# Optimization experiments

Measured on AMD Instinct MI355X. Metric: run time of the kernel, lower is better.

Reference implementation:

```python
import math
import jax, jax.numpy as jnp
import numpy as np

B, NQ, NK, DIM, H, HD = 2, 1024, 2048, 1024, 16, 64


def setup_inputs() -> dict:
    key = jax.random.key(0)
    ks = jax.random.split(key, 12)
    s = 1.0 / math.sqrt(DIM)
    return {
        "q": jax.random.normal(ks[0], (B, NQ, DIM), jnp.float32),
        "k": jax.random.normal(ks[1], (B, NK, DIM), jnp.float32),
        "v": jax.random.normal(ks[2], (B, NK, DIM), jnp.float32),
        "distances": jax.random.uniform(ks[3], (B, NQ, NK), jnp.float32),
        "attn_mask": jax.random.bernoulli(ks[4], 0.5, (B, NQ, NK)),
        "key_padding_mask_q": jax.random.bernoulli(ks[5], 0.5, (B, NQ)),
        "key_padding_mask_k": jax.random.bernoulli(ks[6], 0.5, (B, NK)),
        "Wq": jax.random.normal(ks[7], (H * HD, DIM), jnp.float32) * s,
        "Wk": jax.random.normal(ks[8], (H * HD, DIM), jnp.float32) * s,
        "Wv": jax.random.normal(ks[9], (H * HD, DIM), jnp.float32) * s,
        "Wo": jax.random.normal(ks[10], (DIM, H * HD), jnp.float32) * s,
        "gate_alpha": jnp.float32(0.1),
    }


def reference(q, k, v, distances, attn_mask, key_padding_mask_q,
              key_padding_mask_k, Wq, Wk, Wv, Wo, gate_alpha):
    bsz, q_len, _ = q.shape
    k_len = k.shape[1]
    neg = jnp.finfo(q.dtype).min

    # projections -> (B, H, N, HD)
    qp = (q @ Wq.T).reshape(bsz, q_len, H, HD).transpose(0, 2, 1, 3)
    kp = (k @ Wk.T).reshape(bsz, k_len, H, HD).transpose(0, 2, 1, 3)
    vp = (v @ Wv.T).reshape(bsz, k_len, H, HD).transpose(0, 2, 1, 3)

    scores = jnp.einsum('bhqd,bhkd->bhqk', qp, kp) / math.sqrt(HD)
    scores = jnp.where(attn_mask[:, None, :, :], scores, neg)
    scores = jnp.where(key_padding_mask_k[:, None, None, :], scores, neg)

    attn = jax.nn.softmax(scores, axis=-1)  # (B,H,NQ,NK)

    # distance gating: mask, batch-mean normalize, exponential gate
    d = distances * attn_mask.astype(distances.dtype)
    d = d * key_padding_mask_k[:, None, :].astype(d.dtype)
    mean = d.sum(axis=(-1, -2)) / (q_len * k_len + 1e-6)
    mean = jnp.maximum(mean, 1e-6)[:, None, None]
    d = d / mean
    alpha = jax.nn.softplus(gate_alpha)
    gate = jnp.exp(-alpha * d)[:, None, :, :]  # (B,1,NQ,NK)

    w = attn * gate
    w = w / (w.sum(axis=-1, keepdims=True) + 1e-6)

    out = jnp.einsum('bhqk,bhkd->bhqd', w, vp)
    out = out.transpose(0, 2, 1, 3).reshape(bsz, q_len, H * HD)
    out = out * key_padding_mask_q[:, :, None].astype(out.dtype)
    return out @ Wo.T
```

## Files before the change

### kernel.cpp

```cpp
#include <hip/hip_runtime.h>
#include <hip/hip_bf16.h>
#include <cfloat>

#define B_   2
#define NQ_  1024
#define NK_  2048
#define H_   16
#define HD_  64
#define VPAD 2176
#define GPAD 2112

typedef float  floatx4 __attribute__((ext_vector_type(4)));
typedef __bf16 bf16x8  __attribute__((ext_vector_type(8)));
typedef __bf16 bf16x4  __attribute__((ext_vector_type(4)));

static __device__ __forceinline__ floatx4 mfma16(bf16x8 a, bf16x8 b, floatx4 c) {
    return __builtin_amdgcn_mfma_f32_16x16x32_bf16(a, b, c, 0, 0, 0);
}

static __device__ __forceinline__ void gl_lds(const __bf16* g, __bf16* lbase,
                                              int lane) {
#if __has_builtin(__builtin_amdgcn_global_load_lds)
    __builtin_amdgcn_global_load_lds(
        (const __attribute__((address_space(1))) void*)g,
        (__attribute__((address_space(3))) void*)lbase, 16, 0, 0);
#else
    *(bf16x8*)(lbase + lane * 8) = *(const bf16x8*)g;
#endif
}

struct CvtArgs {
    const float* src[7];
    __bf16*      dst[7];
};

__global__ __launch_bounds__(256) void cvt_mean_kernel(
    CvtArgs a, const float* __restrict__ dist, const int* __restrict__ amask,
    const int* __restrict__ kpmk, float* __restrict__ msum,
    __bf16* __restrict__ dmask)
{
    if (blockIdx.x >= 1792) {
        const int mb = blockIdx.x - 1792;
        const int b  = mb >> 9;
        const float* d  = dist  + (size_t)b * NQ_ * NK_;
        const int*   am = amask + (size_t)b * NQ_ * NK_;
        const int*   km = kpmk  + b * NK_;
        __bf16*      dm = dmask + (size_t)b * NQ_ * GPAD;
        const int base = (mb & 511) * 256 + threadIdx.x;
        float s = 0.f;
        #pragma unroll
        for (int j = 0; j < 4; j++) {
            const int i   = base + j * 131072;
            const int idx = i * 4;
            const int kk  = idx & (NK_ - 1);
            const int q   = i >> 9;
            float4 dv = *(const float4*)(d + idx);
            int4   mv = *(const int4*)(am + idx);
            int4   kv = *(const int4*)(km + kk);
            bf16x4 o;
            if (mv.x && kv.x) { s += dv.x; o[0] = (__bf16)dv.x; } else o[0] = (__bf16)3e38f;
            if (mv.y && kv.y) { s += dv.y; o[1] = (__bf16)dv.y; } else o[1] = (__bf16)3e38f;
            if (mv.z && kv.z) { s += dv.z; o[2] = (__bf16)dv.z; } else o[2] = (__bf16)3e38f;
            if (mv.w && kv.w) { s += dv.w; o[3] = (__bf16)dv.w; } else o[3] = (__bf16)3e38f;
            *(bf16x4*)&dm[(size_t)q * GPAD + kk] = o;
        }
        #pragma unroll
        for (int off = 32; off >= 1; off >>= 1) s += __shfl_down(s, off);
        __shared__ float wsum[4];
        if ((threadIdx.x & 63) == 0) wsum[threadIdx.x >> 6] = s;
        __syncthreads();
        if (threadIdx.x == 0)
            atomicAdd(&msum[b], wsum[0] + wsum[1] + wsum[2] + wsum[3]);
        return;
    }
    #pragma unroll
    for (int j = 0; j < 4; j++) {
        size_t r = (size_t)blockIdx.x * 1024 + j * 256 + threadIdx.x;
        int s;
        if (r < 262144)                  { s = 0; }
        else if ((r -= 262144) < 524288) { s = 1; }
        else if ((r -= 524288) < 524288) { s = 2; }
        else { r -= 524288; s = 3 + (int)(r >> 17); r &= 131071; }
        const float* sp = a.src[s] + r * 8;
        float4 f0 = *(const float4*)sp;
        float4 f1 = *(const float4*)(sp + 4);
        bf16x8 o;
        o[0] = (__bf16)f0.x; o[1] = (__bf16)f0.y; o[2] = (__bf16)f0.z; o[3] = (__bf16)f0.w;
        o[4] = (__bf16)f1.x; o[5] = (__bf16)f1.y; o[6] = (__bf16)f1.z; o[7] = (__bf16)f1.w;
        *(bf16x8*)(a.dst[s] + r * 8) = o;
    }
}

template <typename EPI>
static __device__ __forceinline__ void gemm128_core(
    const __bf16* __restrict__ A, const __bf16* __restrict__ Bw,
    int m0, int n0, __bf16* As, __bf16* Bs, EPI epi)
{
    const int t    = threadIdx.x;
    const int w    = t >> 6, lane = t & 63;
    const int lrow = lane & 15, quad = lane >> 4;
    const int lr   = lane >> 2, lc = lane & 3;

    floatx4 acc[4][4];
    #pragma unroll
    for (int mi = 0; mi < 4; mi++)
        #pragma unroll
        for (int ni = 0; ni < 4; ni++) acc[mi][ni] = floatx4{0.f, 0.f, 0.f, 0.f};

    const __bf16* ga = A  + (size_t)(m0 + w * 32 + lr) * 1024 + lc * 8;
    const __bf16* gb = Bw + (size_t)(n0 + w * 32 + lr) * 1024 + lc * 8;

    for (int k0 = 0; k0 < 1024; k0 += 64) {
        __syncthreads();
        #pragma unroll
        for (int h = 0; h < 2; h++) {
            gl_lds(ga + k0 + h * 32,             &As[h * 4096 + (w * 32) * 32],      lane);
            gl_lds(ga + k0 + h * 32 + 16 * 1024, &As[h * 4096 + (w * 32 + 16) * 32], lane);
            gl_lds(gb + k0 + h * 32,             &Bs[h * 4096 + (w * 32) * 32],      lane);
            gl_lds(gb + k0 + h * 32 + 16 * 1024, &Bs[h * 4096 + (w * 32 + 16) * 32], lane);
        }
        __syncthreads();

        #pragma unroll
        for (int h = 0; h < 2; h++) {
            bf16x8 af[4], bfr[4];
            #pragma unroll
            for (int mi = 0; mi < 4; mi++)
                af[mi] = *(const bf16x8*)
                    &As[h * 4096 + ((w & 1) * 64 + mi * 16 + lrow) * 32 + quad * 8];
            #pragma unroll
            for (int ni = 0; ni < 4; ni++)
                bfr[ni] = *(const bf16x8*)
                    &Bs[h * 4096 + ((w >> 1) * 64 + ni * 16 + lrow) * 32 + quad * 8];
            #pragma unroll
            for (int mi = 0; mi < 4; mi++)
                #pragma unroll
                for (int ni = 0; ni < 4; ni++)
                    acc[mi][ni] = mfma16(af[mi], bfr[ni], acc[mi][ni]);
        }
    }

    #pragma unroll
    for (int mi = 0; mi < 4; mi++)
        #pragma unroll
        for (int ni = 0; ni < 4; ni++)
            #pragma unroll
            for (int r = 0; r < 4; r++) {
                const int m = m0 + (w & 1) * 64 + mi * 16 + quad * 4 + r;
                const int n = n0 + (w >> 1) * 64 + ni * 16 + lrow;
                epi(m, n, acc[mi][ni][r]);
            }
}

template <typename EPI>
static __device__ __forceinline__ void gemm32_core(
    const __bf16* __restrict__ A, const __bf16* __restrict__ Bw,
    int m0, int n0, EPI epi)
{
    __shared__ alignas(16) __bf16 As[2][32 * 32];
    __shared__ alignas(16) __bf16 Bs[2][128 * 32];
    const int t    = threadIdx.x;
    const int w    = t >> 6, lane = t & 63;
    const int lrow = lane & 15, quad = lane >> 4;
    const int lr   = lane >> 2, lc = lane & 3;

    floatx4 acc[2][2];
    #pragma unroll
    for (int mi = 0; mi < 2; mi++)
        #pragma unroll
        for (int ni = 0; ni < 2; ni++) acc[mi][ni] = floatx4{0.f, 0.f, 0.f, 0.f};

    const __bf16* ga = A  + (size_t)(m0 + (w & 1) * 16 + lr) * 1024 + lc * 8;
    const __bf16* gb = Bw + (size_t)(n0 + w * 32 + lr) * 1024 + lc * 8;

    for (int k0 = 0; k0 < 1024; k0 += 64) {
        __syncthreads();
        #pragma unroll
        for (int h = 0; h < 2; h++) {
            if (w < 2)
                gl_lds(ga + k0 + h * 32, &As[h][(w * 16) * 32], lane);
            gl_lds(gb + k0 + h * 32,             &Bs[h][(w * 32) * 32],      lane);
            gl_lds(gb + k0 + h * 32 + 16 * 1024, &Bs[h][(w * 32 + 16) * 32], lane);
        }
        __syncthreads();

        #pragma unroll
        for (int h = 0; h < 2; h++) {
            bf16x8 af[2], bfr[2];
            #pragma unroll
            for (int mi = 0; mi < 2; mi++)
                af[mi] = *(const bf16x8*)
                    &As[h][(mi * 16 + lrow) * 32 + quad * 8];
            #pragma unroll
            for (int ni = 0; ni < 2; ni++)
                bfr[ni] = *(const bf16x8*)
                    &Bs[h][(w * 32 + ni * 16 + lrow) * 32 + quad * 8];
            #pragma unroll
            for (int mi = 0; mi < 2; mi++)
                #pragma unroll
                for (int ni = 0; ni < 2; ni++)
                    acc[mi][ni] = mfma16(af[mi], bfr[ni], acc[mi][ni]);
        }
    }

    #pragma unroll
    for (int mi = 0; mi < 2; mi++)
        #pragma unroll
        for (int ni = 0; ni < 2; ni++)
            #pragma unroll
            for (int r = 0; r < 4; r++) {
                const int m = m0 + mi * 16 + quad * 4 + r;
                const int n = n0 + w * 32 + ni * 16 + lrow;
                epi(m, n, acc[mi][ni][r]);
            }
}

__global__ __launch_bounds__(256) void proj_kernel(
    const __bf16* __restrict__ qb, const __bf16* __restrict__ kb,
    const __bf16* __restrict__ vb, const __bf16* __restrict__ wqb,
    const __bf16* __restrict__ wkb, const __bf16* __restrict__ wvb,
    __bf16* __restrict__ qp, __bf16* __restrict__ kp,
    __bf16* __restrict__ vpT)
{
    __shared__ alignas(16) __bf16 As[2 * 128 * 32];
    __shared__ alignas(16) __bf16 Bs[2 * 128 * 32];
    const int z = blockIdx.z;
    if (z == 0) {
        if ((int)blockIdx.x >= 16) return;
        gemm128_core(qb, wqb, blockIdx.x * 128, blockIdx.y * 128, As, Bs,
                     [&](int m, int n, float v) {
            const int b = m >> 10, q = m & 1023;
            const int h = n >> 6,  d = n & 63;
            qp[(((size_t)(b * 16 + h) * NQ_ + q) << 6) + d] = (__bf16)v;
        });
    } else if (z == 1) {
        gemm128_core(kb, wkb, blockIdx.x * 128, blockIdx.y * 128, As, Bs,
                     [&](int m, int n, float v) {
            const int b = m >> 11, key = m & 2047;
            const int h = n >> 6,  d = n & 63;
            kp[(((size_t)(b * 16 + h) * NK_ + key) << 6) + d] = (__bf16)v;
        });
    } else {
        gemm128_core(wvb, vb, blockIdx.y * 128, blockIdx.x * 128, As, Bs,
                     [&](int m, int n, float v) {
            const int h = m >> 6,  d = m & 63;
            const int b = n >> 11, key = n & 2047;
            vpT[((size_t)(b * 16 + h) * HD_ + d) * VPAD + key] = (__bf16)v;
        });
    }
}

__global__ __launch_bounds__(256) void oproj_kernel(
    const __bf16* __restrict__ A, const __bf16* __restrict__ W,
    float* __restrict__ Cout)
{
    const int m0 = blockIdx.x * 32, n0 = blockIdx.y * 128;
    gemm32_core(A, W, m0, n0, [&](int m, int n, float v) {
        Cout[(size_t)m * 1024 + n] = v;
    });
}

__global__ __launch_bounds__(256, 4) void attn_kernel(
    const __bf16* __restrict__ qp, const __bf16* __restrict__ kp,
    const __bf16* __restrict__ vpT, const __bf16* __restrict__ dmask,
    const float* __restrict__ msum, const float* __restrict__ galpha,
    float* __restrict__ Opart, float* __restrict__ Gpart)
{
    __shared__ __bf16 Ks[64 * 72];
    __shared__ __bf16 Vt[2][64 * 72];
    __shared__ __bf16 Ps[4][16 * 72];
    const int t    = threadIdx.x;
    const int w    = t >> 6, lane = t & 63;
    const int lrow = lane & 15, quad = lane >> 4;
    const int bid  = ((blockIdx.x & 7) << 7) | (blockIdx.x >> 3);
    const int qt   = bid & 15;
    const int bh   = (bid >> 4) & 31;
    const int z    = bid >> 9;
    const int b    = bh >> 4, h = bh & 15;
    const int q0   = qt * 64 + w * 16;
    const int kb0  = z * (NK_ / 2);
    const int NT   = NK_ / 128;

    const float mean  = fmaxf(msum[b] / ((float)(NQ_ * NK_) + 1e-6f), 1e-6f);
    const float alpha = log1pf(__expf(galpha[0]));
    const float cg    = -alpha / mean;

    const __bf16* qb = qp + ((size_t)bh * NQ_ + q0 + lrow) * HD_ + quad * 8;
    const bf16x8 qf0 = *(const bf16x8*)qb;
    const bf16x8 qf1 = *(const bf16x8*)(qb + 32);

    const int srow0 = t >> 3,        sc0 = t & 7;
    const int srow1 = 32 + (t >> 3), sc1 = t & 7;
    const int so0 = srow0 * 72 + sc0 * 8;
    const int so1 = srow1 * 72 + sc1 * 8;
    const __bf16* Kg = kp  + ((size_t)bh * NK_ + kb0) * HD_;
    const __bf16* Vg = vpT + (size_t)bh * HD_ * VPAD + kb0;
    const __bf16* grow = dmask + ((size_t)b * NQ_ + q0 + lrow) * GPAD + kb0;

    float G = 0.f;
    floatx4 O[4];
    #pragma unroll
    for (int nb = 0; nb < 4; nb++) O[nb] = floatx4{0.f, 0.f, 0.f, 0.f};

    bf16x8 kr0, kr1, vr0, vr1;
    bf16x4 gr[4];
    auto loadt = [&](int kb) {
        kr0 = *(const bf16x8*)(Kg + (size_t)(kb + srow0) * HD_ + sc0 * 8);
        kr1 = *(const bf16x8*)(Kg + (size_t)(kb + srow1) * HD_ + sc1 * 8);
        vr0 = *(const bf16x8*)(Vg + (size_t)srow0 * VPAD + kb + sc0 * 8);
        vr1 = *(const bf16x8*)(Vg + (size_t)srow1 * VPAD + kb + sc1 * 8);
        #pragma unroll
        for (int c = 0; c < 4; c++)
            gr[c] = *(const bf16x4*)(grow + kb + c * 16 + quad * 4);
    };
    loadt(0);

    for (int ib = 0; ib < NT; ib++) {
        const int kb  = ib * 64;
        const int cur = ib & 1;

        __syncthreads();
        *(bf16x8*)&Ks[so0]      = kr0;
        *(bf16x8*)&Ks[so1]      = kr1;
        *(bf16x8*)&Vt[cur][so0] = vr0;
        *(bf16x8*)&Vt[cur][so1] = vr1;
        __syncthreads();

        bf16x4 gcur[4];
        #pragma unroll
        for (int c = 0; c < 4; c++) gcur[c] = gr[c];
        if (ib + 1 < NT) loadt(kb + 64);

        __builtin_amdgcn_s_setprio(1);
        floatx4 s4[4];
        #pragma unroll
        for (int c = 0; c < 4; c++) {
            bf16x8 kf0 = *(const bf16x8*)&Ks[(c * 16 + lrow) * 72 + quad * 8];
            bf16x8 kf1 = *(const bf16x8*)&Ks[(c * 16 + lrow) * 72 + 32 + quad * 8];
            floatx4 a = floatx4{0.f, 0.f, 0.f, 0.f};
            a = mfma16(kf0, qf0, a);
            a = mfma16(kf1, qf1, a);
            s4[c] = a;
        }

        if (ib > 0) {
            const int prv = cur ^ 1;
            bf16x8 pf0 = *(const bf16x8*)&Ps[w][lrow * 72 + quad * 8];
            bf16x8 pf1 = *(const bf16x8*)&Ps[w][lrow * 72 + 32 + quad * 8];
            #pragma unroll
            for (int nb = 0; nb < 4; nb++) {
                bf16x8 vf0 = *(const bf16x8*)
                    &Vt[prv][(nb * 16 + lrow) * 72 + quad * 8];
                bf16x8 vf1 = *(const bf16x8*)
                    &Vt[prv][(nb * 16 + lrow) * 72 + 32 + quad * 8];
                O[nb] = mfma16(pf0, vf0, O[nb]);
                O[nb] = mfma16(pf1, vf1, O[nb]);
            }
        }
        __builtin_amdgcn_s_setprio(0);

        #pragma unroll
        for (int c = 0; c < 4; c++) {
            const float e0 = __expf(fmaf(s4[c][0], 0.125f, cg * (float)gcur[c][0]));
            const float e1 = __expf(fmaf(s4[c][1], 0.125f, cg * (float)gcur[c][1]));
            const float e2 = __expf(fmaf(s4[c][2], 0.125f, cg * (float)gcur[c][2]));
            const float e3 = __expf(fmaf(s4[c][3], 0.125f, cg * (float)gcur[c][3]));
            G += (e0 + e1) + (e2 + e3);
            bf16x4 pk;
            pk[0] = (__bf16)e0; pk[1] = (__bf16)e1;
            pk[2] = (__bf16)e2; pk[3] = (__bf16)e3;
            *(bf16x4*)&Ps[w][lrow * 72 + c * 16 + quad * 4] = pk;
        }
    }

    {
        const int prv = (NT - 1) & 1;
        bf16x8 pf0 = *(const bf16x8*)&Ps[w][lrow * 72 + quad * 8];
        bf16x8 pf1 = *(const bf16x8*)&Ps[w][lrow * 72 + 32 + quad * 8];
        #pragma unroll
        for (int nb = 0; nb < 4; nb++) {
            bf16x8 vf0 = *(const bf16x8*)&Vt[prv][(nb * 16 + lrow) * 72 + quad * 8];
            bf16x8 vf1 = *(const bf16x8*)&Vt[prv][(nb * 16 + lrow) * 72 + 32 + quad * 8];
            O[nb] = mfma16(pf0, vf0, O[nb]);
            O[nb] = mfma16(pf1, vf1, O[nb]);
        }
    }

    G += __shfl_xor(G, 16);
    G += __shfl_xor(G, 32);

    float* Op = Opart + (size_t)z * (B_ * NQ_ * 1024)
                      + ((size_t)b * NQ_ + q0) * 1024 + h * HD_;
    #pragma unroll
    for (int r = 0; r < 4; r++) {
        const int qr = quad * 4 + r;
        #pragma unroll
        for (int nb = 0; nb < 4; nb++)
            Op[(size_t)qr * 1024 + nb * 16 + lrow] = O[nb][r];
    }
    if (lane < 16)
        Gpart[(size_t)z * (32 * 1024) + bh * 1024 + q0 + lane] = G;
}

__global__ __launch_bounds__(256) void combine_kernel(
    const float* __restrict__ Opart, const float* __restrict__ Gpart,
    const int* __restrict__ kpmq, __bf16* __restrict__ attnout)
{
    const int idx = blockIdx.x * 256 + threadIdx.x;
    const int m   = idx >> 8;
    const int c4  = (idx & 255) * 4;
    const int b   = m >> 10, q = m & 1023;
    const int h   = c4 >> 6;
    const float g = Gpart[(b * 16 + h) * 1024 + q]
                  + Gpart[32 * 1024 + (b * 16 + h) * 1024 + q];
    const float f = kpmq[b * NQ_ + q] ? 1.f / (g + 1e-30f) : 0.f;
    const float4 o0 = *(const float4*)(Opart + (size_t)m * 1024 + c4);
    const float4 o1 = *(const float4*)(Opart + (size_t)(B_ * NQ_) * 1024
                                              + (size_t)m * 1024 + c4);
    bf16x4 r;
    r[0] = (__bf16)((o0.x + o1.x) * f);
    r[1] = (__bf16)((o0.y + o1.y) * f);
    r[2] = (__bf16)((o0.z + o1.z) * f);
    r[3] = (__bf16)((o0.w + o1.w) * f);
    *(bf16x4*)&attnout[(size_t)m * 1024 + c4] = r;
}

extern "C" void kernel_launch(void* const* d_in, const int* in_sizes, int n_in,
                              void* d_out, int out_size, void* d_ws,
                              size_t ws_size, hipStream_t stream)
{
    const float* q      = (const float*)d_in[0];
    const float* k      = (const float*)d_in[1];
    const float* v      = (const float*)d_in[2];
    const float* dist   = (const float*)d_in[3];
    const int*   amask  = (const int*)d_in[4];
    const int*   kpmq   = (const int*)d_in[5];
    const int*   kpmk   = (const int*)d_in[6];
    const float* Wq     = (const float*)d_in[7];
    const float* Wk     = (const float*)d_in[8];
    const float* Wv     = (const float*)d_in[9];
    const float* Wo     = (const float*)d_in[10];
    const float* galpha = (const float*)d_in[11];

    char* p = (char*)d_ws;
    float*  msum = (float*)p;                 p += 256;
    __bf16* qb   = (__bf16*)p;                p += (size_t)2097152 * 2;
    __bf16* kb   = (__bf16*)p;                p += (size_t)4194304 * 2;
    __bf16* vb   = (__bf16*)p;                p += (size_t)4194304 * 2;
    __bf16* wqb  = (__bf16*)p;                p += (size_t)1048576 * 2;
    __bf16* wkb  = (__bf16*)p;                p += (size_t)1048576 * 2;
    __bf16* wvb  = (__bf16*)p;                p += (size_t)1048576 * 2;
    __bf16* wob  = (__bf16*)p;                p += (size_t)1048576 * 2;
    __bf16* qp   = (__bf16*)p;                p += (size_t)2097152 * 2;
    __bf16* kpb  = (__bf16*)p;                p += (size_t)4194304 * 2;
    __bf16* vpT  = (__bf16*)p;                p += (size_t)32 * 64 * VPAD * 2;
    __bf16* dmask = (__bf16*)p;               p += (size_t)2048 * GPAD * 2;
    __bf16* attnout = (__bf16*)p;             p += (size_t)2097152 * 2;

    float* Opart = (float*)kb;
    float* Gpart = (float*)qb;

    CvtArgs ca;
    ca.src[0] = q;  ca.src[1] = k;  ca.src[2] = v;
    ca.src[3] = Wq; ca.src[4] = Wk; ca.src[5] = Wv; ca.src[6] = Wo;
    ca.dst[0] = qb;  ca.dst[1] = kb;  ca.dst[2] = vb;
    ca.dst[3] = wqb; ca.dst[4] = wkb; ca.dst[5] = wvb; ca.dst[6] = wob;

    hipMemsetAsync(msum, 0, 256, stream);
    cvt_mean_kernel<<<2816, 256, 0, stream>>>(ca, dist, amask, kpmk, msum,
                                              dmask);
    proj_kernel<<<dim3(32, 8, 3), 256, 0, stream>>>(qb, kb, vb, wqb, wkb, wvb,
                                                    qp, kpb, vpT);
    attn_kernel<<<1024, 256, 0, stream>>>(qp, kpb, vpT, dmask,
                                          msum, galpha, Opart, Gpart);
    combine_kernel<<<2048, 256, 0, stream>>>(Opart, Gpart, kpmq, attnout);
    oproj_kernel<<<dim3(64, 8), 256, 0, stream>>>(attnout, wob, (float*)d_out);
}
```

Measured before the change: 250.9 us.

## Load V fragments directly to registers and double-buffer K in LDS

V tiles are no longer staged through shared memory. Each wave loads its MFMA B-operand fragments for V straight from global memory into registers. K gets a double-buffered LDS array so the next tile is written after the QK MFMAs, which removes one of the two barriers per iteration. This cuts LDS traffic and synchronisation. In exchange each wave issues redundant global V loads (no sharing across the four waves) and holds more registers, which may pressure occupancy at launch bounds of 4.

```diff
diff --git a/kernel.cpp b/kernel.cpp
--- a/kernel.cpp
+++ b/kernel.cpp
@@ -266,8 +266,7 @@
     const float* __restrict__ msum, const float* __restrict__ galpha,
     float* __restrict__ Opart, float* __restrict__ Gpart)
 {
-    __shared__ __bf16 Ks[64 * 72];
-    __shared__ __bf16 Vt[2][64 * 72];
+    __shared__ __bf16 Ks[2][64 * 72];
     __shared__ __bf16 Ps[4][16 * 72];
     const int t    = threadIdx.x;
     const int w    = t >> 6, lane = t & 63;
@@ -302,62 +301,75 @@
     #pragma unroll
     for (int nb = 0; nb < 4; nb++) O[nb] = floatx4{0.f, 0.f, 0.f, 0.f};
 
-    bf16x8 kr0, kr1, vr0, vr1;
+    bf16x8 kr0, kr1;
     bf16x4 gr[4];
-    auto loadt = [&](int kb) {
+    bf16x8 vr0[4], vr1[4];
+
+    auto loadK = [&](int kb) {
         kr0 = *(const bf16x8*)(Kg + (size_t)(kb + srow0) * HD_ + sc0 * 8);
         kr1 = *(const bf16x8*)(Kg + (size_t)(kb + srow1) * HD_ + sc1 * 8);
-        vr0 = *(const bf16x8*)(Vg + (size_t)srow0 * VPAD + kb + sc0 * 8);
-        vr1 = *(const bf16x8*)(Vg + (size_t)srow1 * VPAD + kb + sc1 * 8);
+    };
+    auto writeK = [&](int buf) {
+        *(bf16x8*)&Ks[buf][so0] = kr0;
+        *(bf16x8*)&Ks[buf][so1] = kr1;
+    };
+    auto loadG = [&](int kb) {
         #pragma unroll
         for (int c = 0; c < 4; c++)
             gr[c] = *(const bf16x4*)(grow + kb + c * 16 + quad * 4);
     };
-    loadt(0);
+    auto loadV = [&](int kb) {
+        #pragma unroll
+        for (int nb = 0; nb < 4; nb++) {
+            const __bf16* vrow = Vg + (size_t)(nb * 16 + lrow) * VPAD + kb;
+            vr0[nb] = *(const bf16x8*)(vrow + quad * 8);
+            vr1[nb] = *(const bf16x8*)(vrow + 32 + quad * 8);
+        }
+    };
+
+    loadK(0);
+    writeK(0);
+    loadK(64);
+    loadG(0);
+    loadV(0);
 
     for (int ib = 0; ib < NT; ib++) {
         const int kb  = ib * 64;
         const int cur = ib & 1;
 
         __syncthreads();
-        *(bf16x8*)&Ks[so0]      = kr0;
-        *(bf16x8*)&Ks[so1]      = kr1;
-        *(bf16x8*)&Vt[cur][so0] = vr0;
-        *(bf16x8*)&Vt[cur][so1] = vr1;
-        __syncthreads();
-
-        bf16x4 gcur[4];
-        #pragma unroll
-        for (int c = 0; c < 4; c++) gcur[c] = gr[c];
-        if (ib + 1 < NT) loadt(kb + 64);
 
         __builtin_amdgcn_s_setprio(1);
         floatx4 s4[4];
         #pragma unroll
         for (int c = 0; c < 4; c++) {
-            bf16x8 kf0 = *(const bf16x8*)&Ks[(c * 16 + lrow) * 72 + quad * 8];
-            bf16x8 kf1 = *(const bf16x8*)&Ks[(c * 16 + lrow) * 72 + 32 + quad * 8];
+            bf16x8 kf0 = *(const bf16x8*)&Ks[cur][(c * 16 + lrow) * 72 + quad * 8];
+            bf16x8 kf1 = *(const bf16x8*)&Ks[cur][(c * 16 + lrow) * 72 + 32 + quad * 8];
             floatx4 a = floatx4{0.f, 0.f, 0.f, 0.f};
             a = mfma16(kf0, qf0, a);
             a = mfma16(kf1, qf1, a);
             s4[c] = a;
         }
 
+        if (ib + 1 < NT) writeK(cur ^ 1);
+
         if (ib > 0) {
-            const int prv = cur ^ 1;
             bf16x8 pf0 = *(const bf16x8*)&Ps[w][lrow * 72 + quad * 8];
             bf16x8 pf1 = *(const bf16x8*)&Ps[w][lrow * 72 + 32 + quad * 8];
             #pragma unroll
             for (int nb = 0; nb < 4; nb++) {
-                bf16x8 vf0 = *(const bf16x8*)
-                    &Vt[prv][(nb * 16 + lrow) * 72 + quad * 8];
-                bf16x8 vf1 = *(const bf16x8*)
-                    &Vt[prv][(nb * 16 + lrow) * 72 + 32 + quad * 8];
-                O[nb] = mfma16(pf0, vf0, O[nb]);
-                O[nb] = mfma16(pf1, vf1, O[nb]);
+                O[nb] = mfma16(pf0, vr0[nb], O[nb]);
+                O[nb] = mfma16(pf1, vr1[nb], O[nb]);
             }
         }
         __builtin_amdgcn_s_setprio(0);
+
+        bf16x4 gcur[4];
+        #pragma unroll
+        for (int c = 0; c < 4; c++) gcur[c] = gr[c];
+        if (ib > 0)      loadV(kb);
+        if (ib + 2 < NT) loadK(kb + 128);
+        if (ib + 1 < NT) loadG(kb + 64);
 
         #pragma unroll
         for (int c = 0; c < 4; c++) {
@@ -374,15 +386,12 @@
     }
 
     {
-        const int prv = (NT - 1) & 1;
         bf16x8 pf0 = *(const bf16x8*)&Ps[w][lrow * 72 + quad * 8];
         bf16x8 pf1 = *(const bf16x8*)&Ps[w][lrow * 72 + 32 + quad * 8];
         #pragma unroll
         for (int nb = 0; nb < 4; nb++) {
-            bf16x8 vf0 = *(const bf16x8*)&Vt[prv][(nb * 16 + lrow) * 72 + quad * 8];
-            bf16x8 vf1 = *(const bf16x8*)&Vt[prv][(nb * 16 + lrow) * 72 + 32 + quad * 8];
-            O[nb] = mfma16(pf0, vf0, O[nb]);
-            O[nb] = mfma16(pf1, vf1, O[nb]);
+            O[nb] = mfma16(pf0, vr0[nb], O[nb]);
+            O[nb] = mfma16(pf1, vr1[nb], O[nb]);
         }
     }
 
```

Result: slower. 299.0 us (+19.2%).
